# Kernel tuning notes

Measured on AMD Instinct MI355X. Metric: run time of the kernel, lower is better.

## Reference

```python
import jax, jax.numpy as jnp
import numpy as np

N = 100_000   # nodes
E = 1_600_000 # edges per edge type
DIN = 128     # input_dim
DH = 128      # prot_hidden_dim
L = 3         # prot_num_layers
EPS = 1e-5


def setup_inputs() -> dict:
    key = jax.random.key(0)
    ks = jax.random.split(key, 8)
    s = 1.0 / np.sqrt(DH)
    return {
        "x": jax.random.normal(ks[0], (N, DIN), jnp.float32),
        "src": jax.random.randint(ks[1], (3, E), 0, N, jnp.int32),
        "dst": jax.random.randint(ks[2], (3, E), 0, N, jnp.int32),
        "gc_W0": jax.random.normal(ks[3], (3, DIN, DH), jnp.float32) * s,
        "gc_b0": jnp.zeros((3, DH), jnp.float32),
        "gc_W": jax.random.normal(ks[4], (L - 1, 3, DH, DH), jnp.float32) * s,
        "gc_b": jnp.zeros((L - 1, 3, DH), jnp.float32),
        "fc_W": jax.random.normal(ks[5], (L, DH, DH), jnp.float32) * s,
        "fc_b": jnp.zeros((L, DH), jnp.float32),
        "bn_gamma": jnp.ones((L, DH), jnp.float32),
        "bn_beta": jnp.zeros((L, DH), jnp.float32),
    }


def _graph_conv(x, src, dst, W, b):
    # DGL GraphConv, norm='both': D_in^{-1/2} A D_out^{-1/2} X W + b
    ones = jnp.ones(src.shape[0], x.dtype)
    deg_out = jnp.clip(jax.ops.segment_sum(ones, src, num_segments=N), 1.0)
    deg_in = jnp.clip(jax.ops.segment_sum(ones, dst, num_segments=N), 1.0)
    # apply weight first (same math; keeps gathered message width = DH)
    h = (x * jax.lax.rsqrt(deg_out)[:, None]) @ W  # [N, DH]
    agg = jax.ops.segment_sum(h[src], dst, num_segments=N)  # gather + scatter-add
    return agg * jax.lax.rsqrt(deg_in)[:, None] + b


def _batchnorm(x, gamma, beta):
    # training-mode BatchNorm1d: biased batch statistics
    mu = jnp.mean(x, axis=0)
    var = jnp.mean(jnp.square(x - mu), axis=0)
    return (x - mu) * jax.lax.rsqrt(var + EPS) * gamma + beta


def reference(x, src, dst, gc_W0, gc_b0, gc_W, gc_b, fc_W, fc_b, bn_gamma, bn_beta):
    h = x
    for l in range(L):
        W = gc_W0 if l == 0 else gc_W[l - 1]
        b = gc_b0 if l == 0 else gc_b[l - 1]
        # HeteroGraphConv with aggregate='sum' over 3 edge types
        out = _graph_conv(h, src[0], dst[0], W[0], b[0])
        for e in range(1, 3):
            out = out + _graph_conv(h, src[e], dst[e], W[e], b[e])
        # FC -> ReLU -> BatchNorm (dropout = identity in eval mode)
        h = _batchnorm(jax.nn.relu(out @ fc_W[l] + fc_b[l]), bn_gamma[l], bn_beta[l])
    return h
```

## Files before the change

### kernel.cpp

```cpp
#include <hip/hip_runtime.h>


#define EPSV 1e-5f
#define CH 4096
#define MAXNB 512

typedef _Float16 h2v __attribute__((ext_vector_type(2)));
typedef _Float16 f16x8 __attribute__((ext_vector_type(8)));
typedef __attribute__((ext_vector_type(4))) float f4v;

__global__ void coarse_hist(const int* __restrict__ src, const int* __restrict__ dst,
                            int* __restrict__ bhd, int* __restrict__ bhs,
                            int E, int NB, int nblk) {
    __shared__ int hd[MAXNB], hs[MAXNB];
    const int t = blockIdx.y;
    const int blk = blockIdx.x;
    for (int i = threadIdx.x; i < MAXNB; i += 256) { hd[i] = 0; hs[i] = 0; }
    __syncthreads();
    int base = blk * CH;
    int end = base + CH < E ? base + CH : E;
    const int* sp = src + (size_t)t * E;
    const int* dp = dst + (size_t)t * E;
    for (int i = base + threadIdx.x; i < end; i += 256) {
        atomicAdd(&hd[dp[i] >> 8], 1);
        atomicAdd(&hs[sp[i] >> 8], 1);
    }
    __syncthreads();
    for (int b = threadIdx.x; b < NB; b += 256) {
        size_t o = (size_t)(t * NB + b) * nblk + blk;
        bhd[o] = hd[b];
        bhs[o] = hs[b];
    }
}

__global__ void blk_scan(const int* __restrict__ bhd, const int* __restrict__ bhs,
                         int* __restrict__ bpd, int* __restrict__ bps,
                         int* __restrict__ chd, int* __restrict__ chs,
                         int NB, int nblk) {
    __shared__ int s[MAXNB];
    const int half = 3 * NB;
    const int id = blockIdx.x;
    const bool isS = id >= half;
    const int r = isS ? id - half : id;
    const int* cnt = isS ? bhs : bhd;
    int* pfx = isS ? bps : bpd;
    int* tot = isS ? chs : chd;
    const size_t base = (size_t)r * nblk;
    const int tid = threadIdx.x;
    int v0 = (tid < nblk) ? cnt[base + tid] : 0;
    int v1 = (tid + 256 < nblk) ? cnt[base + tid + 256] : 0;
    s[tid] = v0;
    s[tid + 256] = v1;
    __syncthreads();
    for (int o = 1; o < MAXNB; o <<= 1) {
        int a0 = s[tid], a1 = s[tid + 256];
        int p0 = (tid >= o) ? s[tid - o] : 0;
        int p1 = s[tid + 256 - o];
        __syncthreads();
        s[tid] = a0 + p0;
        s[tid + 256] = a1 + p1;
        __syncthreads();
    }
    if (tid < nblk) pfx[base + tid] = s[tid] - v0;
    if (tid + 256 < nblk) pfx[base + tid + 256] = s[tid + 256] - v1;
    if (tid == 0) tot[r] = s[nblk - 1];
}

__global__ void scan_off(const int* __restrict__ chd, const int* __restrict__ chs,
                         int* __restrict__ offd, int* __restrict__ offs,
                         int* __restrict__ rowptr, int NB, int N, int E) {
    __shared__ int s[MAXNB];
    int tid = threadIdx.x;
    for (int a = 0; a < 6; ++a) {
        const int* h = (a < 3) ? chd + a * NB : chs + (a - 3) * NB;
        int* off = (a < 3) ? offd + a * (NB + 1) : offs + (a - 3) * (NB + 1);
        s[tid] = (tid < NB) ? h[tid] : 0;
        __syncthreads();
        for (int o = 1; o < MAXNB; o <<= 1) {
            int v = (tid >= o) ? s[tid - o] : 0;
            __syncthreads();
            s[tid] += v;
            __syncthreads();
        }
        if (tid < NB) {
            off[tid + 1] = s[tid];
            if (tid == 0) off[0] = 0;
        }
        __syncthreads();
    }
    if (tid < 3) rowptr[tid * (N + 1) + N] = E;
}

__launch_bounds__(256)
__global__ void scatter_coarse(const int* __restrict__ src, const int* __restrict__ dst,
                               const int* __restrict__ bhd, const int* __restrict__ bhs,
                               const int* __restrict__ bpd, const int* __restrict__ bps,
                               const int* __restrict__ offd, const int* __restrict__ offs,
                               int* __restrict__ dbuf, unsigned char* __restrict__ sbuf,
                               int E, int NB, int nblk) {
    __shared__ int hd[MAXNB], hs[MAXNB];
    __shared__ int lod[MAXNB], los[MAXNB];
    __shared__ int bd[MAXNB], bs[MAXNB];
    __shared__ int rbi[CH];
    __shared__ unsigned char rbs[CH];
    const int tid = threadIdx.x;
    const int t = blockIdx.y;
    const int blk = blockIdx.x;
    const int base = blk * CH;
    const int end = base + CH < E ? base + CH : E;
    const int cnt = end - base;
    const int* sp = src + (size_t)t * E;
    const int* dp = dst + (size_t)t * E;

    for (int b = tid; b < MAXNB; b += 256) {
        if (b < NB) {
            size_t o = (size_t)(t * NB + b) * nblk + blk;
            int cd = bhd[o], cs2 = bhs[o];
            hd[b] = cd;
            hs[b] = cs2;
            bd[b] = offd[t * (NB + 1) + b] + bpd[o];
            bs[b] = offs[t * (NB + 1) + b] + bps[o];
        } else {
            hd[b] = 0;
            hs[b] = 0;
        }
    }
    lod[tid] = hd[tid]; lod[tid + 256] = hd[tid + 256];
    los[tid] = hs[tid]; los[tid + 256] = hs[tid + 256];
    __syncthreads();
    for (int o = 1; o < MAXNB; o <<= 1) {
        int a0 = lod[tid], a1 = lod[tid + 256];
        int b0 = los[tid], b1 = los[tid + 256];
        int p0 = (tid >= o) ? lod[tid - o] : 0;
        int p1 = lod[tid + 256 - o];
        int q0 = (tid >= o) ? los[tid - o] : 0;
        int q1 = los[tid + 256 - o];
        __syncthreads();
        lod[tid] = a0 + p0; lod[tid + 256] = a1 + p1;
        los[tid] = b0 + q0; los[tid + 256] = b1 + q1;
        __syncthreads();
    }
    hd[tid] = lod[tid] - hd[tid]; hd[tid + 256] = lod[tid + 256] - hd[tid + 256];
    hs[tid] = los[tid] - hs[tid]; hs[tid + 256] = los[tid + 256] - hs[tid + 256];
    __syncthreads();
    for (int i = base + tid; i < end; i += 256) {
        int sv = sp[i], dv = dp[i];
        int lp = atomicAdd(&hd[dv >> 8], 1);
        rbi[lp] = (sv << 8) | (dv & 255);
        int ls = atomicAdd(&hs[sv >> 8], 1);
        rbs[ls] = (unsigned char)(sv & 255);
    }
    __syncthreads();
    for (int i = tid; i < cnt; i += 256) {
        int lo = 0, hi = NB - 1;
        while (lo < hi) { int mid = (lo + hi) >> 1; if (lod[mid] > i) hi = mid; else lo = mid + 1; }
        int excl = lo ? lod[lo - 1] : 0;
        dbuf[(size_t)t * E + bd[lo] + (i - excl)] = rbi[i];
    }
    for (int i = tid; i < cnt; i += 256) {
        int lo = 0, hi = NB - 1;
        while (lo < hi) { int mid = (lo + hi) >> 1; if (los[mid] > i) hi = mid; else lo = mid + 1; }
        int excl = lo ? los[lo - 1] : 0;
        sbuf[(size_t)t * E + bs[lo] + (i - excl)] = rbs[i];
    }
}

__global__ void fine_src(const unsigned char* __restrict__ sbuf, const int* __restrict__ offs,
                         float* __restrict__ dro, int E, int N, int NB) {
    __shared__ int h[256];
    int b = blockIdx.x, t = blockIdx.y;
    int tid = threadIdx.x;
    h[tid] = 0;
    __syncthreads();
    int beg = offs[t * (NB + 1) + b], end = offs[t * (NB + 1) + b + 1];
    const unsigned char* sp = sbuf + (size_t)t * E;
    for (int i = beg + tid; i < end; i += 256) atomicAdd(&h[sp[i]], 1);
    __syncthreads();
    int node = b * 256 + tid;
    if (node < N) {
        int dg = h[tid] < 1 ? 1 : h[tid];
        dro[(size_t)t * N + node] = rsqrtf((float)dg);
    }
}

#define FDCAP 6656
__global__ void fine_dst(const int* __restrict__ dbuf, const int* __restrict__ offd,
                         const float* __restrict__ dro, int* __restrict__ erec,
                         int* __restrict__ rowptr, float* __restrict__ dri,
                         int E, int N, int NB) {
    __shared__ int h[256], sc[256], cur[256];
    __shared__ int rb[FDCAP];
    int b = blockIdx.x, t = blockIdx.y;
    int tid = threadIdx.x;
    h[tid] = 0;
    __syncthreads();
    int beg = offd[t * (NB + 1) + b], end = offd[t * (NB + 1) + b + 1];
    int cnt = end - beg;
    const int* dp = dbuf + (size_t)t * E;
    const float* drt = dro + (size_t)t * N;
    for (int i = beg + tid; i < end; i += 256) atomicAdd(&h[dp[i] & 255], 1);
    __syncthreads();
    sc[tid] = h[tid];
    __syncthreads();
    for (int o = 1; o < 256; o <<= 1) {
        int v = (tid >= o) ? sc[tid - o] : 0;
        __syncthreads();
        sc[tid] += v;
        __syncthreads();
    }
    int excl = sc[tid] - h[tid];
    cur[tid] = excl;
    int node = b * 256 + tid;
    if (node < N) {
        rowptr[t * (N + 1) + node] = beg + excl;
        int dg = h[tid] < 1 ? 1 : h[tid];
        dri[(size_t)t * N + node] = rsqrtf((float)dg);
    }
    __syncthreads();
    if (cnt <= FDCAP) {
        for (int i = beg + tid; i < end; i += 256) {
            int v = dp[i];
            int p = atomicAdd(&cur[v & 255], 1);
            rb[p] = v >> 8;
        }
        __syncthreads();
        for (int i = tid; i < cnt; i += 256) {
            int sv = rb[i];
            int wq = (int)(drt[sv] * 4095.0f + 0.5f);
            erec[(size_t)t * E + beg + i] = sv | (wq << 20);
        }
    } else {
        for (int i = beg + tid; i < end; i += 256) {
            int v = dp[i];
            int sv = v >> 8;
            int wq = (int)(drt[sv] * 4095.0f + 0.5f);
            int p = beg + atomicAdd(&cur[v & 255], 1);
            erec[(size_t)t * E + p] = sv | (wq << 20);
        }
    }
}

__device__ __forceinline__ h2v ash2(unsigned u) {
    union { unsigned u; h2v h; } c;
    c.u = u;
    return c.h;
}
__device__ __forceinline__ unsigned packh2(float lo, float hi) {
    union { h2v h; unsigned u; } c;
    c.h = (h2v){(_Float16)lo, (_Float16)hi};
    return c.u;
}
__device__ __forceinline__ unsigned short f16b(float f) {
    union { _Float16 h; unsigned short s; } c;
    c.h = (_Float16)f;
    return c.s;
}

__global__ void cvt_f16(const float* __restrict__ h, unsigned short* __restrict__ h2,
                        int total8) {
    int i = blockIdx.x * 256 + threadIdx.x;
    if (i >= total8) return;
    const float4* hp = (const float4*)h + (size_t)i * 2;
    float4 v0 = hp[0], v1 = hp[1];
    uint4 o;
    o.x = packh2(v0.x, v0.y);
    o.y = packh2(v0.z, v0.w);
    o.z = packh2(v1.x, v1.y);
    o.w = packh2(v1.z, v1.w);
    ((uint4*)h2)[i] = o;
}

__global__ void pack_w(const float* __restrict__ gcW0, const float* __restrict__ gcW,
                       const float* __restrict__ fcW, unsigned short* __restrict__ Wg,
                       unsigned short* __restrict__ Wf) {
    int mat = blockIdx.x;
    const float* srcp;
    unsigned short* dstp;
    if (mat < 9) {
        int l = mat / 3, e = mat % 3;
        srcp = (l == 0) ? gcW0 + (size_t)e * 16384
                        : gcW + ((size_t)(l - 1) * 3 + e) * 16384;
        dstp = Wg + (size_t)mat * 16384;
    } else {
        srcp = fcW + (size_t)(mat - 9) * 16384;
        dstp = Wf + (size_t)(mat - 9) * 16384;
    }
    for (int p = threadIdx.x; p < 16384; p += 256) {
        int j = p & 7;
        int ln = (p >> 3) & 63;
        int nt = (p >> 9) & 7;
        int ks = p >> 12;
        int k = ks * 32 + (ln >> 4) * 8 + j;
        int n = nt * 16 + (ln & 15);
        dstp[p] = f16b(srcp[k * 128 + n]);
    }
}

template <int AFF>
__launch_bounds__(256)
__global__ void agg_kernel(const unsigned short* __restrict__ h2, const int* __restrict__ rowptrB,
                           const int* __restrict__ erecB, const float* __restrict__ driB,
                           const float* __restrict__ bnsum, const float* __restrict__ gamma,
                           const float* __restrict__ beta, float invn,
                           unsigned short* __restrict__ zB, int N, int E) {
    __shared__ float lss[256];
    if (AFF) {
        int tid = threadIdx.x;
        if (tid < 128) {
            float mean = bnsum[tid] * invn;
            float var = bnsum[128 + tid] * invn - mean * mean;
            float sc = gamma[tid] * rsqrtf(var + EPSV);
            lss[tid] = sc;
            lss[128 + tid] = beta[tid] - mean * sc;
        }
        __syncthreads();
    }
    const int e = blockIdx.y;
    const int* rowptr = rowptrB + e * (N + 1);
    const int* erec = erecB + (size_t)e * E;
    const float* dri = driB + (size_t)e * N;
    unsigned short* z = zB + (size_t)e * N * 128;

    int idx = blockIdx.x * 256 + threadIdx.x;
    int node = idx >> 4;
    int lq = idx & 15;
    if (node >= N) return;
    int beg = rowptr[node], end = rowptr[node + 1];
    const uint4* hp = (const uint4*)h2 + lq;
    h2v ac0 = (h2v)0, ac1 = (h2v)0, ac2 = (h2v)0, ac3 = (h2v)0;
    float wacc = 0.f;
    const float IW = 1.0f / 4095.0f;

    int j = beg;
    for (; j + 8 <= end; j += 8) {
        int r[8];
#pragma unroll
        for (int q = 0; q < 8; ++q) r[q] = erec[j + q];
        uint4 u[8];
#pragma unroll
        for (int q = 0; q < 8; ++q) u[q] = hp[(size_t)(r[q] & 0xFFFFF) * 16];
#pragma unroll
        for (int q = 0; q < 8; ++q) {
            float wf = (float)((unsigned)r[q] >> 20) * IW;
            if (AFF) wacc += wf;
            _Float16 wh = (_Float16)wf;
            h2v wp = (h2v){wh, wh};
            ac0 = ash2(u[q].x) * wp + ac0;
            ac1 = ash2(u[q].y) * wp + ac1;
            ac2 = ash2(u[q].z) * wp + ac2;
            ac3 = ash2(u[q].w) * wp + ac3;
        }
    }
    for (; j + 4 <= end; j += 4) {
        int r[4];
#pragma unroll
        for (int q = 0; q < 4; ++q) r[q] = erec[j + q];
        uint4 u[4];
#pragma unroll
        for (int q = 0; q < 4; ++q) u[q] = hp[(size_t)(r[q] & 0xFFFFF) * 16];
#pragma unroll
        for (int q = 0; q < 4; ++q) {
            float wf = (float)((unsigned)r[q] >> 20) * IW;
            if (AFF) wacc += wf;
            _Float16 wh = (_Float16)wf;
            h2v wp = (h2v){wh, wh};
            ac0 = ash2(u[q].x) * wp + ac0;
            ac1 = ash2(u[q].y) * wp + ac1;
            ac2 = ash2(u[q].z) * wp + ac2;
            ac3 = ash2(u[q].w) * wp + ac3;
        }
    }
    for (; j < end; ++j) {
        int r0 = erec[j];
        float wf = (float)((unsigned)r0 >> 20) * IW;
        if (AFF) wacc += wf;
        _Float16 wh = (_Float16)wf;
        h2v wp = (h2v){wh, wh};
        uint4 u0 = hp[(size_t)(r0 & 0xFFFFF) * 16];
        ac0 = ash2(u0.x) * wp + ac0;
        ac1 = ash2(u0.y) * wp + ac1;
        ac2 = ash2(u0.z) * wp + ac2;
        ac3 = ash2(u0.w) * wp + ac3;
    }
    float a0 = (float)ac0[0], a1 = (float)ac0[1];
    float a2 = (float)ac1[0], a3 = (float)ac1[1];
    float a4 = (float)ac2[0], a5 = (float)ac2[1];
    float a6 = (float)ac3[0], a7 = (float)ac3[1];
    float scl = dri[node];
    if (AFF) {
        const float* ap = &lss[lq * 8];
        const float* bp = &lss[128 + lq * 8];
        a0 = ap[0] * a0 + bp[0] * wacc;
        a1 = ap[1] * a1 + bp[1] * wacc;
        a2 = ap[2] * a2 + bp[2] * wacc;
        a3 = ap[3] * a3 + bp[3] * wacc;
        a4 = ap[4] * a4 + bp[4] * wacc;
        a5 = ap[5] * a5 + bp[5] * wacc;
        a6 = ap[6] * a6 + bp[6] * wacc;
        a7 = ap[7] * a7 + bp[7] * wacc;
    }
    uint4 o;
    o.x = packh2(a0 * scl, a1 * scl);
    o.y = packh2(a2 * scl, a3 * scl);
    o.z = packh2(a4 * scl, a5 * scl);
    o.w = packh2(a6 * scl, a7 * scl);
    ((uint4*)z)[(size_t)node * 16 + lq] = o;
}

template <int MODE>
__launch_bounds__(512)
__global__ void mfma_layer(const unsigned short* __restrict__ zB,
                           const unsigned short* __restrict__ Wgp,
                           const float* __restrict__ b3,
                           const unsigned short* __restrict__ Wfp,
                           const float* __restrict__ fcb,
                           unsigned short* __restrict__ outb, float* __restrict__ outf,
                           float* __restrict__ bnsum, int M) {
    __shared__ unsigned short T[128 * 128];
    __shared__ float red[256];
    const int tid = threadIdx.x;
    const int l = tid & 63;
    const int wv = tid >> 6;
    const int wm = wv >> 1;
    const int wn = wv & 1;
    const int m0 = blockIdx.x * 128;
    const int lr = l & 15;
    const int lk = (l >> 4) * 8;

    int rowb[2];
#pragma unroll
    for (int mt = 0; mt < 2; ++mt) {
        int r = m0 + wm * 32 + mt * 16 + lr;
        rowb[mt] = (r < M) ? r : (M - 1);
    }

    {
        f4v acc[2][4];
#pragma unroll
        for (int i = 0; i < 2; ++i)
#pragma unroll
            for (int j = 0; j < 4; ++j) acc[i][j] = (f4v){0.f, 0.f, 0.f, 0.f};
#pragma unroll
        for (int e = 0; e < 3; ++e) {
            const unsigned short* zp = zB + (size_t)e * M * 128;
            const unsigned short* wp = Wgp + (size_t)e * 16384;
#pragma unroll
            for (int ks = 0; ks < 4; ++ks) {
                f16x8 a[2], b[4];
#pragma unroll
                for (int mt = 0; mt < 2; ++mt)
                    a[mt] = *(const f16x8*)(zp + (size_t)rowb[mt] * 128 + ks * 32 + lk);
#pragma unroll
                for (int nt = 0; nt < 4; ++nt)
                    b[nt] = *(const f16x8*)(wp + ks * 4096 + (wn * 4 + nt) * 512 + l * 8);
#pragma unroll
                for (int mt = 0; mt < 2; ++mt)
#pragma unroll
                    for (int nt = 0; nt < 4; ++nt)
                        acc[mt][nt] = __builtin_amdgcn_mfma_f32_16x16x32_f16(
                            a[mt], b[nt], acc[mt][nt], 0, 0, 0);
            }
        }
        float bs[4];
        int col[4];
#pragma unroll
        for (int nt = 0; nt < 4; ++nt) {
            col[nt] = wn * 64 + nt * 16 + lr;
            bs[nt] = b3[col[nt]] + b3[128 + col[nt]] + b3[256 + col[nt]];
        }
#pragma unroll
        for (int mt = 0; mt < 2; ++mt) {
#pragma unroll
            for (int r = 0; r < 4; ++r) {
                int rl = wm * 32 + mt * 16 + (l >> 4) * 4 + r;
#pragma unroll
                for (int nt = 0; nt < 4; ++nt) {
                    int c = col[nt];
                    int chunk = (c >> 3) ^ (rl & 15);
                    T[rl * 128 + chunk * 8 + (c & 7)] = f16b(acc[mt][nt][r] + bs[nt]);
                }
            }
        }
    }
    __syncthreads();

    f4v acc2[2][4];
#pragma unroll
    for (int i = 0; i < 2; ++i)
#pragma unroll
        for (int j = 0; j < 4; ++j) acc2[i][j] = (f4v){0.f, 0.f, 0.f, 0.f};
#pragma unroll
    for (int ks = 0; ks < 4; ++ks) {
        f16x8 a[2], b[4];
#pragma unroll
        for (int mt = 0; mt < 2; ++mt) {
            int rl = wm * 32 + mt * 16 + lr;
            int chunk = (ks * 4 + (l >> 4)) ^ lr;
            a[mt] = *(const f16x8*)&T[rl * 128 + chunk * 8];
        }
#pragma unroll
        for (int nt = 0; nt < 4; ++nt)
            b[nt] = *(const f16x8*)(Wfp + ks * 4096 + (wn * 4 + nt) * 512 + l * 8);
#pragma unroll
        for (int mt = 0; mt < 2; ++mt)
#pragma unroll
            for (int nt = 0; nt < 4; ++nt)
                acc2[mt][nt] = __builtin_amdgcn_mfma_f32_16x16x32_f16(
                    a[mt], b[nt], acc2[mt][nt], 0, 0, 0);
    }

    float bv[4], cs[4] = {}, cq[4] = {};
    int col[4];
#pragma unroll
    for (int nt = 0; nt < 4; ++nt) {
        col[nt] = wn * 64 + nt * 16 + lr;
        bv[nt] = fcb[col[nt]];
    }
#pragma unroll
    for (int mt = 0; mt < 2; ++mt) {
#pragma unroll
        for (int r = 0; r < 4; ++r) {
            int row = m0 + wm * 32 + mt * 16 + (l >> 4) * 4 + r;
            if (row < M) {
#pragma unroll
                for (int nt = 0; nt < 4; ++nt) {
                    float v = acc2[mt][nt][r] + bv[nt];
                    v = v > 0.f ? v : 0.f;
                    cs[nt] += v;
                    cq[nt] += v * v;
                    if (MODE == 0)
                        outb[(size_t)row * 128 + col[nt]] = f16b(v);
                    else
                        outf[(size_t)row * 128 + col[nt]] = v;
                }
            }
        }
    }
    if (tid < 256) red[tid] = 0.f;
    __syncthreads();
#pragma unroll
    for (int nt = 0; nt < 4; ++nt) {
        atomicAdd(&red[col[nt]], cs[nt]);
        atomicAdd(&red[128 + col[nt]], cq[nt]);
    }
    __syncthreads();
    if (tid < 128) {
        atomicAdd(&bnsum[tid], red[tid]);
        atomicAdd(&bnsum[128 + tid], red[128 + tid]);
    }
}

__global__ void bn_apply(float* __restrict__ h, const float* __restrict__ bnsum,
                         const float* __restrict__ gamma, const float* __restrict__ beta,
                         float invn, int total4) {
    __shared__ float lss[256];
    int tid = threadIdx.x;
    if (tid < 128) {
        float mean = bnsum[tid] * invn;
        float var = bnsum[128 + tid] * invn - mean * mean;
        float sc = gamma[tid] * rsqrtf(var + EPSV);
        lss[tid] = sc;
        lss[128 + tid] = beta[tid] - mean * sc;
    }
    __syncthreads();
    int i = blockIdx.x * 256 + tid;
    if (i >= total4) return;
    int c4 = (i & 31) * 4;
    float4 sc = *(const float4*)&lss[c4];
    float4 sh = *(const float4*)&lss[128 + c4];
    float4 v = ((float4*)h)[i];
    v.x = v.x * sc.x + sh.x;
    v.y = v.y * sc.y + sh.y;
    v.z = v.z * sc.z + sh.z;
    v.w = v.w * sc.w + sh.w;
    ((float4*)h)[i] = v;
}

extern "C" void kernel_launch(void* const* d_in, const int* in_sizes, int n_in,
                              void* d_out, int out_size, void* d_ws, size_t ws_size,
                              hipStream_t stream) {
    const float* x    = (const float*)d_in[0];
    const int*   src  = (const int*)d_in[1];
    const int*   dst  = (const int*)d_in[2];
    const float* gcW0 = (const float*)d_in[3];
    const float* gcb0 = (const float*)d_in[4];
    const float* gcW  = (const float*)d_in[5];
    const float* gcb  = (const float*)d_in[6];
    const float* fcW  = (const float*)d_in[7];
    const float* fcb  = (const float*)d_in[8];
    const float* bng  = (const float*)d_in[9];
    const float* bnb  = (const float*)d_in[10];
    float* out = (float*)d_out;

    const int N = in_sizes[0] / 128;
    const int E = in_sizes[1] / 3;
    const int NB = (N + 255) / 256;
    const int nblk = (E + CH - 1) / CH;

    char* w = (char*)d_ws;
    auto alloc = [&](size_t bytes) -> char* {
        char* p = w;
        w += (bytes + 255) & ~(size_t)255;
        return p;
    };
    unsigned short* zB    = (unsigned short*)alloc((size_t)3 * N * 128 * 2);
    unsigned short* h2    = (unsigned short*)alloc((size_t)N * 128 * 2);
    unsigned short* Wg    = (unsigned short*)alloc((size_t)9 * 16384 * 2);
    unsigned short* Wf    = (unsigned short*)alloc((size_t)3 * 16384 * 2);
    int*   erec   = (int*)alloc((size_t)3 * E * 4);
    int*   rowptr = (int*)alloc((size_t)3 * (N + 1) * 4);
    float* dro    = (float*)alloc((size_t)3 * N * 4);
    float* dri    = (float*)alloc((size_t)3 * N * 4);
    int*   bhd    = (int*)alloc((size_t)3 * NB * nblk * 4);
    int*   bhs    = (int*)alloc((size_t)3 * NB * nblk * 4);
    int*   bpd    = (int*)alloc((size_t)3 * NB * nblk * 4);
    int*   bps    = (int*)alloc((size_t)3 * NB * nblk * 4);
    int*   chd    = (int*)alloc((size_t)3 * NB * 4);
    int*   chs    = (int*)alloc((size_t)3 * NB * 4);
    int*   offd   = (int*)alloc((size_t)3 * (NB + 1) * 4);
    int*   offs   = (int*)alloc((size_t)3 * (NB + 1) * 4);
    float* bnsum  = (float*)alloc(256 * 4);
    int* dbuf = (int*)zB;
    unsigned char* sbuf = (unsigned char*)(dbuf + (size_t)3 * E);

    dim3 cg2(nblk, 3);
    coarse_hist<<<cg2, 256, 0, stream>>>(src, dst, bhd, bhs, E, NB, nblk);
    blk_scan<<<2 * 3 * NB, 256, 0, stream>>>(bhd, bhs, bpd, bps, chd, chs, NB, nblk);
    scan_off<<<1, MAXNB, 0, stream>>>(chd, chs, offd, offs, rowptr, NB, N, E);
    scatter_coarse<<<cg2, 256, 0, stream>>>(src, dst, bhd, bhs, bpd, bps, offd, offs,
                                            dbuf, sbuf, E, NB, nblk);
    dim3 fg(NB, 3);
    fine_src<<<fg, 256, 0, stream>>>(sbuf, offs, dro, E, N, NB);
    fine_dst<<<fg, 256, 0, stream>>>(dbuf, offd, dro, erec, rowptr, dri, E, N, NB);

    pack_w<<<12, 256, 0, stream>>>(gcW0, gcW, fcW, Wg, Wf);
    const int cvtGrid = (N * 16 + 255) / 256;
    cvt_f16<<<cvtGrid, 256, 0, stream>>>(x, h2, N * 16);

    const int gemmGrid = (N + 127) / 128;
    const float invn = 1.0f / (float)N;
    dim3 aggG((N * 16 + 255) / 256, 3);

    for (int l = 0; l < 3; ++l) {
        const float* bl = (l == 0) ? gcb0 : gcb + (size_t)(l - 1) * 3 * 128;
        if (l == 0)
            agg_kernel<0><<<aggG, 256, 0, stream>>>(h2, rowptr, erec, dri,
                                                    nullptr, nullptr, nullptr, invn,
                                                    zB, N, E);
        else
            agg_kernel<1><<<aggG, 256, 0, stream>>>(h2, rowptr, erec, dri,
                                                    bnsum, bng + (size_t)(l - 1) * 128,
                                                    bnb + (size_t)(l - 1) * 128, invn,
                                                    zB, N, E);
        hipMemsetAsync(bnsum, 0, 256 * 4, stream);
        if (l < 2)
            mfma_layer<0><<<gemmGrid, 512, 0, stream>>>(zB, Wg + (size_t)l * 3 * 16384, bl,
                                                        Wf + (size_t)l * 16384,
                                                        fcb + (size_t)l * 128,
                                                        h2, nullptr, bnsum, N);
        else
            mfma_layer<1><<<gemmGrid, 512, 0, stream>>>(zB, Wg + (size_t)l * 3 * 16384, bl,
                                                        Wf + (size_t)l * 16384,
                                                        fcb + (size_t)l * 128,
                                                        nullptr, out, bnsum, N);
    }
    bn_apply<<<(N * 32 + 255) / 256, 256, 0, stream>>>(out, bnsum, bng + 2 * 128,
                                                       bnb + 2 * 128, invn, N * 32);
}
```

Before: 875.4 us.

## Fuse neighbor aggregation with MFMA GEMM per layer via LDS tile

```diff
diff --git a/kernel.cpp b/kernel.cpp
--- a/kernel.cpp
+++ b/kernel.cpp
@@ -296,171 +296,146 @@
     }
 }
 
-template <int AFF>
+template <int AFF, int MODE>
 __launch_bounds__(256)
-__global__ void agg_kernel(const unsigned short* __restrict__ h2, const int* __restrict__ rowptrB,
-                           const int* __restrict__ erecB, const float* __restrict__ driB,
-                           const float* __restrict__ bnsum, const float* __restrict__ gamma,
-                           const float* __restrict__ beta, float invn,
-                           unsigned short* __restrict__ zB, int N, int E) {
+__global__ void fused_layer(const unsigned short* __restrict__ hin,
+                            const int* __restrict__ rowptrB, const int* __restrict__ erecB,
+                            const float* __restrict__ driB,
+                            const float* __restrict__ bnin, const float* __restrict__ gamma,
+                            const float* __restrict__ beta, float invn,
+                            const unsigned short* __restrict__ Wgp, const float* __restrict__ b3,
+                            const unsigned short* __restrict__ Wfp, const float* __restrict__ fcb,
+                            unsigned short* __restrict__ outb, float* __restrict__ outf,
+                            float* __restrict__ bnout, int N, int E) {
+    __shared__ unsigned short T[64 * 128];
+    __shared__ float red[256];
     __shared__ float lss[256];
-    if (AFF) {
-        int tid = threadIdx.x;
-        if (tid < 128) {
-            float mean = bnsum[tid] * invn;
-            float var = bnsum[128 + tid] * invn - mean * mean;
-            float sc = gamma[tid] * rsqrtf(var + EPSV);
-            lss[tid] = sc;
-            lss[128 + tid] = beta[tid] - mean * sc;
-        }
-        __syncthreads();
-    }
-    const int e = blockIdx.y;
-    const int* rowptr = rowptrB + e * (N + 1);
-    const int* erec = erecB + (size_t)e * E;
-    const float* dri = driB + (size_t)e * N;
-    unsigned short* z = zB + (size_t)e * N * 128;
-
-    int idx = blockIdx.x * 256 + threadIdx.x;
-    int node = idx >> 4;
-    int lq = idx & 15;
-    if (node >= N) return;
-    int beg = rowptr[node], end = rowptr[node + 1];
-    const uint4* hp = (const uint4*)h2 + lq;
-    h2v ac0 = (h2v)0, ac1 = (h2v)0, ac2 = (h2v)0, ac3 = (h2v)0;
-    float wacc = 0.f;
-    const float IW = 1.0f / 4095.0f;
-
-    int j = beg;
-    for (; j + 8 <= end; j += 8) {
-        int r[8];
-#pragma unroll
-        for (int q = 0; q < 8; ++q) r[q] = erec[j + q];
-        uint4 u[8];
-#pragma unroll
-        for (int q = 0; q < 8; ++q) u[q] = hp[(size_t)(r[q] & 0xFFFFF) * 16];
-#pragma unroll
-        for (int q = 0; q < 8; ++q) {
-            float wf = (float)((unsigned)r[q] >> 20) * IW;
-            if (AFF) wacc += wf;
-            _Float16 wh = (_Float16)wf;
-            h2v wp = (h2v){wh, wh};
-            ac0 = ash2(u[q].x) * wp + ac0;
-            ac1 = ash2(u[q].y) * wp + ac1;
-            ac2 = ash2(u[q].z) * wp + ac2;
-            ac3 = ash2(u[q].w) * wp + ac3;
-        }
-    }
-    for (; j + 4 <= end; j += 4) {
-        int r[4];
-#pragma unroll
-        for (int q = 0; q < 4; ++q) r[q] = erec[j + q];
-        uint4 u[4];
-#pragma unroll
-        for (int q = 0; q < 4; ++q) u[q] = hp[(size_t)(r[q] & 0xFFFFF) * 16];
-#pragma unroll
-        for (int q = 0; q < 4; ++q) {
-            float wf = (float)((unsigned)r[q] >> 20) * IW;
-            if (AFF) wacc += wf;
-            _Float16 wh = (_Float16)wf;
-            h2v wp = (h2v){wh, wh};
-            ac0 = ash2(u[q].x) * wp + ac0;
-            ac1 = ash2(u[q].y) * wp + ac1;
-            ac2 = ash2(u[q].z) * wp + ac2;
-            ac3 = ash2(u[q].w) * wp + ac3;
-        }
-    }
-    for (; j < end; ++j) {
-        int r0 = erec[j];
-        float wf = (float)((unsigned)r0 >> 20) * IW;
-        if (AFF) wacc += wf;
-        _Float16 wh = (_Float16)wf;
-        h2v wp = (h2v){wh, wh};
-        uint4 u0 = hp[(size_t)(r0 & 0xFFFFF) * 16];
-        ac0 = ash2(u0.x) * wp + ac0;
-        ac1 = ash2(u0.y) * wp + ac1;
-        ac2 = ash2(u0.z) * wp + ac2;
-        ac3 = ash2(u0.w) * wp + ac3;
-    }
-    float a0 = (float)ac0[0], a1 = (float)ac0[1];
-    float a2 = (float)ac1[0], a3 = (float)ac1[1];
-    float a4 = (float)ac2[0], a5 = (float)ac2[1];
-    float a6 = (float)ac3[0], a7 = (float)ac3[1];
-    float scl = dri[node];
-    if (AFF) {
-        const float* ap = &lss[lq * 8];
-        const float* bp = &lss[128 + lq * 8];
-        a0 = ap[0] * a0 + bp[0] * wacc;
-        a1 = ap[1] * a1 + bp[1] * wacc;
-        a2 = ap[2] * a2 + bp[2] * wacc;
-        a3 = ap[3] * a3 + bp[3] * wacc;
-        a4 = ap[4] * a4 + bp[4] * wacc;
-        a5 = ap[5] * a5 + bp[5] * wacc;
-        a6 = ap[6] * a6 + bp[6] * wacc;
-        a7 = ap[7] * a7 + bp[7] * wacc;
-    }
-    uint4 o;
-    o.x = packh2(a0 * scl, a1 * scl);
-    o.y = packh2(a2 * scl, a3 * scl);
-    o.z = packh2(a4 * scl, a5 * scl);
-    o.w = packh2(a6 * scl, a7 * scl);
-    ((uint4*)z)[(size_t)node * 16 + lq] = o;
-}
-
-template <int MODE>
-__launch_bounds__(512)
-__global__ void mfma_layer(const unsigned short* __restrict__ zB,
-                           const unsigned short* __restrict__ Wgp,
-                           const float* __restrict__ b3,
-                           const unsigned short* __restrict__ Wfp,
-                           const float* __restrict__ fcb,
-                           unsigned short* __restrict__ outb, float* __restrict__ outf,
-                           float* __restrict__ bnsum, int M) {
-    __shared__ unsigned short T[128 * 128];
-    __shared__ float red[256];
     const int tid = threadIdx.x;
     const int l = tid & 63;
     const int wv = tid >> 6;
     const int wm = wv >> 1;
     const int wn = wv & 1;
-    const int m0 = blockIdx.x * 128;
+    const int m0 = blockIdx.x * 64;
     const int lr = l & 15;
-    const int lk = (l >> 4) * 8;
-
-    int rowb[2];
-#pragma unroll
-    for (int mt = 0; mt < 2; ++mt) {
-        int r = m0 + wm * 32 + mt * 16 + lr;
-        rowb[mt] = (r < M) ? r : (M - 1);
+    const float IW = 1.0f / 4095.0f;
+
+    if (AFF) {
+        if (tid < 128) {
+            float mean = bnin[tid] * invn;
+            float var = bnin[128 + tid] * invn - mean * mean;
+            float sc = gamma[tid] * rsqrtf(var + EPSV);
+            lss[tid] = sc;
+            lss[128 + tid] = beta[tid] - mean * sc;
+        }
+        __syncthreads();
+    }
+
+    f4v acc[2][4];
+#pragma unroll
+    for (int i = 0; i < 2; ++i)
+#pragma unroll
+        for (int j = 0; j < 4; ++j) acc[i][j] = (f4v){0.f, 0.f, 0.f, 0.f};
+
+    const int g = tid >> 4;
+    const int lq = tid & 15;
+
+    for (int e = 0; e < 3; ++e) {
+        const int* rowptr = rowptrB + e * (N + 1);
+        const int* erec = erecB + (size_t)e * E;
+        const float* dri = driB + (size_t)e * N;
+        const uint4* hp = (const uint4*)hin + lq;
+
+        for (int b = 0; b < 4; ++b) {
+            int nl = g + 16 * b;
+            int node = m0 + nl;
+            uint4 o = make_uint4(0, 0, 0, 0);
+            if (node < N) {
+                int beg = rowptr[node], end = rowptr[node + 1];
+                h2v ac0 = (h2v)0, ac1 = (h2v)0, ac2 = (h2v)0, ac3 = (h2v)0;
+                float wacc = 0.f;
+                int j = beg;
+                for (; j + 8 <= end; j += 8) {
+                    int r[8];
+#pragma unroll
+                    for (int q = 0; q < 8; ++q) r[q] = erec[j + q];
+                    uint4 u[8];
+#pragma unroll
+                    for (int q = 0; q < 8; ++q) u[q] = hp[(size_t)(r[q] & 0xFFFFF) * 16];
+#pragma unroll
+                    for (int q = 0; q < 8; ++q) {
+                        float wf = (float)((unsigned)r[q] >> 20) * IW;
+                        if (AFF) wacc += wf;
+                        _Float16 wh = (_Float16)wf;
+                        h2v wp = (h2v){wh, wh};
+                        ac0 = ash2(u[q].x) * wp + ac0;
+                        ac1 = ash2(u[q].y) * wp + ac1;
+                        ac2 = ash2(u[q].z) * wp + ac2;
+                        ac3 = ash2(u[q].w) * wp + ac3;
+                    }
+                }
+                for (; j < end; ++j) {
+                    int r0 = erec[j];
+                    float wf = (float)((unsigned)r0 >> 20) * IW;
+                    if (AFF) wacc += wf;
+                    _Float16 wh = (_Float16)wf;
+                    h2v wp = (h2v){wh, wh};
+                    uint4 u0 = hp[(size_t)(r0 & 0xFFFFF) * 16];
+                    ac0 = ash2(u0.x) * wp + ac0;
+                    ac1 = ash2(u0.y) * wp + ac1;
+                    ac2 = ash2(u0.z) * wp + ac2;
+                    ac3 = ash2(u0.w) * wp + ac3;
+                }
+                float a0 = (float)ac0[0], a1 = (float)ac0[1];
+                float a2 = (float)ac1[0], a3 = (float)ac1[1];
+                float a4 = (float)ac2[0], a5 = (float)ac2[1];
+                float a6 = (float)ac3[0], a7 = (float)ac3[1];
+                float scl = dri[node];
+                if (AFF) {
+                    const float* ap = &lss[lq * 8];
+                    const float* bp = &lss[128 + lq * 8];
+                    a0 = ap[0] * a0 + bp[0] * wacc;
+                    a1 = ap[1] * a1 + bp[1] * wacc;
+                    a2 = ap[2] * a2 + bp[2] * wacc;
+                    a3 = ap[3] * a3 + bp[3] * wacc;
+                    a4 = ap[4] * a4 + bp[4] * wacc;
+                    a5 = ap[5] * a5 + bp[5] * wacc;
+                    a6 = ap[6] * a6 + bp[6] * wacc;
+                    a7 = ap[7] * a7 + bp[7] * wacc;
+                }
+                o.x = packh2(a0 * scl, a1 * scl);
+                o.y = packh2(a2 * scl, a3 * scl);
+                o.z = packh2(a4 * scl, a5 * scl);
+                o.w = packh2(a6 * scl, a7 * scl);
+            }
+            int cp = (lq ^ (nl & 15)) * 8;
+            *(uint4*)&T[nl * 128 + cp] = o;
+        }
+        __syncthreads();
+
+        const unsigned short* wp = Wgp + (size_t)e * 16384;
+#pragma unroll
+        for (int ks = 0; ks < 4; ++ks) {
+            f16x8 a[2], b[4];
+#pragma unroll
+            for (int mt = 0; mt < 2; ++mt) {
+                int rl = wm * 32 + mt * 16 + lr;
+                int chunk = (ks * 4 + (l >> 4)) ^ lr;
+                a[mt] = *(const f16x8*)&T[rl * 128 + chunk * 8];
+            }
+#pragma unroll
+            for (int nt = 0; nt < 4; ++nt)
+                b[nt] = *(const f16x8*)(wp + ks * 4096 + (wn * 4 + nt) * 512 + l * 8);
+#pragma unroll
+            for (int mt = 0; mt < 2; ++mt)
+#pragma unroll
+                for (int nt = 0; nt < 4; ++nt)
+                    acc[mt][nt] = __builtin_amdgcn_mfma_f32_16x16x32_f16(
+                        a[mt], b[nt], acc[mt][nt], 0, 0, 0);
+        }
+        __syncthreads();
     }
 
     {
-        f4v acc[2][4];
-#pragma unroll
-        for (int i = 0; i < 2; ++i)
-#pragma unroll
-            for (int j = 0; j < 4; ++j) acc[i][j] = (f4v){0.f, 0.f, 0.f, 0.f};
-#pragma unroll
-        for (int e = 0; e < 3; ++e) {
-            const unsigned short* zp = zB + (size_t)e * M * 128;
-            const unsigned short* wp = Wgp + (size_t)e * 16384;
-#pragma unroll
-            for (int ks = 0; ks < 4; ++ks) {
-                f16x8 a[2], b[4];
-#pragma unroll
-                for (int mt = 0; mt < 2; ++mt)
-                    a[mt] = *(const f16x8*)(zp + (size_t)rowb[mt] * 128 + ks * 32 + lk);
-#pragma unroll
-                for (int nt = 0; nt < 4; ++nt)
-                    b[nt] = *(const f16x8*)(wp + ks * 4096 + (wn * 4 + nt) * 512 + l * 8);
-#pragma unroll
-                for (int mt = 0; mt < 2; ++mt)
-#pragma unroll
-                    for (int nt = 0; nt < 4; ++nt)
-                        acc[mt][nt] = __builtin_amdgcn_mfma_f32_16x16x32_f16(
-                            a[mt], b[nt], acc[mt][nt], 0, 0, 0);
-            }
-        }
         float bs[4];
         int col[4];
 #pragma unroll
@@ -521,7 +496,7 @@
 #pragma unroll
         for (int r = 0; r < 4; ++r) {
             int row = m0 + wm * 32 + mt * 16 + (l >> 4) * 4 + r;
-            if (row < M) {
+            if (row < N) {
 #pragma unroll
                 for (int nt = 0; nt < 4; ++nt) {
                     float v = acc2[mt][nt][r] + bv[nt];
@@ -536,7 +511,7 @@
             }
         }
     }
-    if (tid < 256) red[tid] = 0.f;
+    red[tid] = 0.f;
     __syncthreads();
 #pragma unroll
     for (int nt = 0; nt < 4; ++nt) {
@@ -545,8 +520,8 @@
     }
     __syncthreads();
     if (tid < 128) {
-        atomicAdd(&bnsum[tid], red[tid]);
-        atomicAdd(&bnsum[128 + tid], red[128 + tid]);
+        atomicAdd(&bnout[tid], red[tid]);
+        atomicAdd(&bnout[128 + tid], red[128 + tid]);
     }
 }
 
@@ -603,14 +578,16 @@
         w += (bytes + 255) & ~(size_t)255;
         return p;
     };
-    unsigned short* zB    = (unsigned short*)alloc((size_t)3 * N * 128 * 2);
-    unsigned short* h2    = (unsigned short*)alloc((size_t)N * 128 * 2);
+    unsigned short* hA    = (unsigned short*)alloc((size_t)N * 128 * 2);
+    unsigned short* hB    = (unsigned short*)alloc((size_t)N * 128 * 2);
     unsigned short* Wg    = (unsigned short*)alloc((size_t)9 * 16384 * 2);
     unsigned short* Wf    = (unsigned short*)alloc((size_t)3 * 16384 * 2);
     int*   erec   = (int*)alloc((size_t)3 * E * 4);
     int*   rowptr = (int*)alloc((size_t)3 * (N + 1) * 4);
     float* dro    = (float*)alloc((size_t)3 * N * 4);
     float* dri    = (float*)alloc((size_t)3 * N * 4);
+    int*   dbuf   = (int*)alloc((size_t)3 * E * 4);
+    unsigned char* sbuf = (unsigned char*)alloc((size_t)3 * E);
     int*   bhd    = (int*)alloc((size_t)3 * NB * nblk * 4);
     int*   bhs    = (int*)alloc((size_t)3 * NB * nblk * 4);
     int*   bpd    = (int*)alloc((size_t)3 * NB * nblk * 4);
@@ -619,9 +596,7 @@
     int*   chs    = (int*)alloc((size_t)3 * NB * 4);
     int*   offd   = (int*)alloc((size_t)3 * (NB + 1) * 4);
     int*   offs   = (int*)alloc((size_t)3 * (NB + 1) * 4);
-    float* bnsum  = (float*)alloc(256 * 4);
-    int* dbuf = (int*)zB;
-    unsigned char* sbuf = (unsigned char*)(dbuf + (size_t)3 * E);
+    float* bnsum  = (float*)alloc(3 * 256 * 4);
 
     dim3 cg2(nblk, 3);
     coarse_hist<<<cg2, 256, 0, stream>>>(src, dst, bhd, bhs, E, NB, nblk);
@@ -635,35 +610,26 @@
 
     pack_w<<<12, 256, 0, stream>>>(gcW0, gcW, fcW, Wg, Wf);
     const int cvtGrid = (N * 16 + 255) / 256;
-    cvt_f16<<<cvtGrid, 256, 0, stream>>>(x, h2, N * 16);
-
-    const int gemmGrid = (N + 127) / 128;
+    cvt_f16<<<cvtGrid, 256, 0, stream>>>(x, hA, N * 16);
+    hipMemsetAsync(bnsum, 0, 3 * 256 * 4, stream);
+
+    const int grid = (N + 63) / 64;
     const float invn = 1.0f / (float)N;
-    dim3 aggG((N * 16 + 255) / 256, 3);
-
-    for (int l = 0; l < 3; ++l) {
-        const float* bl = (l == 0) ? gcb0 : gcb + (size_t)(l - 1) * 3 * 128;
-        if (l == 0)
-            agg_kernel<0><<<aggG, 256, 0, stream>>>(h2, rowptr, erec, dri,
-                                                    nullptr, nullptr, nullptr, invn,
-                                                    zB, N, E);
-        else
-            agg_kernel<1><<<aggG, 256, 0, stream>>>(h2, rowptr, erec, dri,
-                                                    bnsum, bng + (size_t)(l - 1) * 128,
-                                                    bnb + (size_t)(l - 1) * 128, invn,
-                                                    zB, N, E);
-        hipMemsetAsync(bnsum, 0, 256 * 4, stream);
-        if (l < 2)
-            mfma_layer<0><<<gemmGrid, 512, 0, stream>>>(zB, Wg + (size_t)l * 3 * 16384, bl,
-                                                        Wf + (size_t)l * 16384,
-                                                        fcb + (size_t)l * 128,
-                                                        h2, nullptr, bnsum, N);
-        else
-            mfma_layer<1><<<gemmGrid, 512, 0, stream>>>(zB, Wg + (size_t)l * 3 * 16384, bl,
-                                                        Wf + (size_t)l * 16384,
-                                                        fcb + (size_t)l * 128,
-                                                        nullptr, out, bnsum, N);
-    }
-    bn_apply<<<(N * 32 + 255) / 256, 256, 0, stream>>>(out, bnsum, bng + 2 * 128,
+
+    fused_layer<0, 0><<<grid, 256, 0, stream>>>(hA, rowptr, erec, dri,
+                                                nullptr, nullptr, nullptr, invn,
+                                                Wg, gcb0, Wf, fcb,
+                                                hB, nullptr, bnsum, N, E);
+    fused_layer<1, 0><<<grid, 256, 0, stream>>>(hB, rowptr, erec, dri,
+                                                bnsum, bng, bnb, invn,
+                                                Wg + (size_t)3 * 16384, gcb,
+                                                Wf + (size_t)16384, fcb + 128,
+                                                hA, nullptr, bnsum + 256, N, E);
+    fused_layer<1, 1><<<grid, 256, 0, stream>>>(hA, rowptr, erec, dri,
+                                                bnsum + 256, bng + 128, bnb + 128, invn,
+                                                Wg + (size_t)6 * 16384, gcb + 3 * 128,
+                                                Wf + (size_t)2 * 16384, fcb + 256,
+                                                nullptr, out, bnsum + 512, N, E);
+    bn_apply<<<(N * 32 + 255) / 256, 256, 0, stream>>>(out, bnsum + 512, bng + 2 * 128,
                                                        bnb + 2 * 128, invn, N * 32);
 }
```

New measurement: 952.7 us. 8.8% more time.
